# Optimization experiments

Hardware: AMD Instinct MI355X
Metric: run time of the kernel (lower is better)

## Reference

```python
import jax, jax.numpy as jnp
import numpy as np

EPS = 1e-5  # BatchNorm eps (ME.MinkowskiBatchNorm default)


def setup_inputs() -> dict:
    key = jax.random.key(0)
    k1, k2, k3, k4 = jax.random.split(key, 4)
    N, Cin, Cout, K = 65536, 256, 128, 8  # K = kernel_size**dimension = 2**3
    x = jax.random.normal(k1, (N, Cin), dtype=jnp.float32)
    W = jax.random.normal(k2, (K, Cin, Cout), dtype=jnp.float32) * 0.02
    gamma = jax.random.uniform(k3, (Cout,), dtype=jnp.float32, minval=0.5, maxval=1.5)
    beta = jax.random.normal(k4, (Cout,), dtype=jnp.float32) * 0.1
    return {"x": x, "W": W, "gamma": gamma, "beta": beta}


def reference(x, W, gamma, beta):
    # Transpose Minkowski conv, kernel=2, stride=2, dim=3: each input voxel
    # emits 2^3 = 8 disjoint child voxels; child for offset k gets x @ W[k].
    # Kernel map is identity per offset (no scatter-add collisions because
    # kernel_size == stride), so outputs stack to [8*N, Cout].
    Cout = W.shape[-1]
    out = jnp.einsum('nc,kcd->knd', x, W).reshape(-1, Cout)  # [8N, Cout]
    # MinkowskiBatchNorm over all active output sites (training batch stats).
    mean = jnp.mean(out, axis=0)
    var = jnp.mean(jnp.square(out - mean), axis=0)  # biased var, as BN uses
    y = (out - mean) * jax.lax.rsqrt(var + EPS) * gamma + beta
    return jnp.maximum(y, 0.0)  # MinkowskiReLU
```

## Files before the change

### kernel.cpp

```cpp
#include <hip/hip_runtime.h>
#include <stdint.h>

#define N_ROWS 65536
#define CIN 256
#define COUT 128

typedef __bf16 bf16x8 __attribute__((ext_vector_type(8)));
typedef float f32x4 __attribute__((ext_vector_type(4)));
typedef unsigned short u16;
typedef unsigned int u32;

__device__ __forceinline__ float truncbf(float f) {
  u32 x = __builtin_bit_cast(u32, f) & 0xFFFF0000u;
  return __builtin_bit_cast(float, x);
}
__device__ __forceinline__ u32 packbf(float a, float b) {
  return __builtin_amdgcn_perm(__builtin_bit_cast(u32, b),
                               __builtin_bit_cast(u32, a), 0x07060302u);
}
__device__ __forceinline__ u32 bf_rne(float f) {
  u32 u = __builtin_bit_cast(u32, f);
  u += 0x7FFFu + ((u >> 16) & 1);
  return u >> 16;
}

__device__ __forceinline__ void async_ld16(const void* g, void* l) {
  __builtin_amdgcn_global_load_lds((const __attribute__((address_space(1))) u32*)g,
                                   (__attribute__((address_space(3))) u32*)l,
                                   16, 0, 0);
}

template <bool EMIT_XB>
__global__ __launch_bounds__(512, 2) void gram_partial(const float* __restrict__ x,
                                                       u32* __restrict__ part,
                                                       float* __restrict__ csb,
                                                       u32* __restrict__ xb,
                                                       const float* __restrict__ W,
                                                       u16* __restrict__ Wt) {
  __shared__ u32 xT[16 * 260];
  __shared__ float cs_s[8][256];
  __shared__ u16 tile[32][128];
  const int tid = threadIdx.x, lane = tid & 63;
  const int w = tid >> 6;
  const int wm = w >> 2, wn = w & 3;
  const int q = lane >> 4, r = lane & 15;
  const int row0 = blockIdx.x * 256;
  const int cq = tid & 63;
  const int np2 = tid >> 6;

  f32x4 acc[8][4];
  #pragma unroll
  for (int i = 0; i < 8; ++i)
    #pragma unroll
    for (int j = 0; j < 4; ++j) acc[i][j] = (f32x4){0.f, 0.f, 0.f, 0.f};
  f32x4 cs = (f32x4){0.f, 0.f, 0.f, 0.f};

  f32x4 a0, a1, b0, b1;
  {
    const int nA = row0 + np2 * 2;
    const int nB = row0 + (np2 + 8) * 2;
    a0 = *(const f32x4*)&x[(size_t)nA * CIN + 4 * cq];
    a1 = *(const f32x4*)&x[(size_t)(nA + 1) * CIN + 4 * cq];
    b0 = *(const f32x4*)&x[(size_t)nB * CIN + 4 * cq];
    b1 = *(const f32x4*)&x[(size_t)(nB + 1) * CIN + 4 * cq];
  }

  for (int ch = 0; ch < 8; ++ch) {
    const int r0 = row0 + ch * 32;
    const int nA = r0 + np2 * 2;
    const int nB = r0 + (np2 + 8) * 2;

    union { u32 d[4]; uint4 v; } pA, pB;
    #pragma unroll
    for (int j = 0; j < 4; ++j) {
      pA.d[j] = packbf(a0[j], a1[j]);
      pB.d[j] = packbf(b0[j], b1[j]);
      cs[j] += truncbf(a0[j]) + truncbf(a1[j]) + truncbf(b0[j]) + truncbf(b1[j]);
    }
    *(uint4*)&xT[np2 * 260 + 4 * cq] = pA.v;
    *(uint4*)&xT[(np2 + 8) * 260 + 4 * cq] = pB.v;
    if (EMIT_XB) {
      uint2 e;
      e.x = packbf(a0[0], a0[1]); e.y = packbf(a0[2], a0[3]);
      *(uint2*)&xb[(size_t)nA * 128 + 2 * cq] = e;
      e.x = packbf(a1[0], a1[1]); e.y = packbf(a1[2], a1[3]);
      *(uint2*)&xb[(size_t)(nA + 1) * 128 + 2 * cq] = e;
      e.x = packbf(b0[0], b0[1]); e.y = packbf(b0[2], b0[3]);
      *(uint2*)&xb[(size_t)nB * 128 + 2 * cq] = e;
      e.x = packbf(b1[0], b1[1]); e.y = packbf(b1[2], b1[3]);
      *(uint2*)&xb[(size_t)(nB + 1) * 128 + 2 * cq] = e;
    }
    f32x4 na0, na1, nb0, nb1;
    if (ch < 7) {
      const int mA = nA + 32, mB = nB + 32;
      na0 = *(const f32x4*)&x[(size_t)mA * CIN + 4 * cq];
      na1 = *(const f32x4*)&x[(size_t)(mA + 1) * CIN + 4 * cq];
      nb0 = *(const f32x4*)&x[(size_t)mB * CIN + 4 * cq];
      nb1 = *(const f32x4*)&x[(size_t)(mB + 1) * CIN + 4 * cq];
    }
    __syncthreads();
    bf16x8 af[8], bfr[4];
    #pragma unroll
    for (int mt = 0; mt < 8; ++mt) {
      int c = wm * 128 + mt * 16 + r;
      union { u32 d[4]; bf16x8 v; } t;
      #pragma unroll
      for (int s = 0; s < 4; ++s) t.d[s] = xT[(4 * q + s) * 260 + c];
      af[mt] = t.v;
    }
    #pragma unroll
    for (int nt = 0; nt < 4; ++nt) {
      int c = wn * 64 + nt * 16 + r;
      union { u32 d[4]; bf16x8 v; } t;
      #pragma unroll
      for (int s = 0; s < 4; ++s) t.d[s] = xT[(4 * q + s) * 260 + c];
      bfr[nt] = t.v;
    }
    #pragma unroll
    for (int mt = 0; mt < 8; ++mt)
      #pragma unroll
      for (int nt = 0; nt < 4; ++nt)
        acc[mt][nt] = __builtin_amdgcn_mfma_f32_16x16x32_bf16(af[mt], bfr[nt], acc[mt][nt], 0, 0, 0);
    __syncthreads();
    if (ch < 7) { a0 = na0; a1 = na1; b0 = nb0; b1 = nb1; }
  }

  u32* pb = part + (size_t)blockIdx.x * 32768;
  #pragma unroll
  for (int mt = 0; mt < 8; ++mt)
    #pragma unroll
    for (int nt = 0; nt < 4; ++nt) {
      int prow = wm * 64 + mt * 8 + q * 2;
      int col = wn * 64 + nt * 16 + r;
      pb[prow * 256 + col] = (bf_rne(acc[mt][nt][1]) << 16) | bf_rne(acc[mt][nt][0]);
      pb[(prow + 1) * 256 + col] = (bf_rne(acc[mt][nt][3]) << 16) | bf_rne(acc[mt][nt][2]);
    }

  *(f32x4*)&cs_s[np2][4 * cq] = cs;
  __syncthreads();
  if (tid < 256) {
    float s = 0.f;
    #pragma unroll
    for (int p = 0; p < 8; ++p) s += cs_s[p][tid];
    csb[(size_t)blockIdx.x * 256 + tid] = s;
  }

  if (blockIdx.x < 64) {
    const int k = blockIdx.x >> 3, cb = blockIdx.x & 7;
    #pragma unroll
    for (int i = 0; i < 2; ++i) {
      int u = tid + i * 512;
      int ci = u >> 5, d4 = (u & 31) * 4;
      float4 f = *(const float4*)&W[((size_t)k * CIN + cb * 32 + ci) * COUT + d4];
      uint2 p; p.x = packbf(f.x, f.y); p.y = packbf(f.z, f.w);
      *(uint2*)&tile[ci][d4] = p;
    }
    __syncthreads();
    {
      int d = tid >> 2, c0 = (tid & 3) * 8;
      union { u16 s[8]; uint4 u4; } p;
      #pragma unroll
      for (int j = 0; j < 8; ++j) p.s[j] = tile[c0 + j][d];
      *(uint4*)&Wt[((size_t)blockIdx.x * 128 + d) * 32 + c0] = p.u4;
    }
  }
}

__global__ __launch_bounds__(256) void gram_reduce(const u32* __restrict__ part,
                                                   float* __restrict__ G) {
  __shared__ float red[16][128];
  const int t = threadIdx.x;
  const int fi = t & 15, grp = t >> 4;
  const int g0 = blockIdx.x * 64;
  const int rp = g0 >> 8, c0 = g0 & 255;
  float fa[4] = {0.f, 0.f, 0.f, 0.f}, fb[4] = {0.f, 0.f, 0.f, 0.f};
  const u32* p = part + (size_t)(grp * 16) * 32768 + g0 + fi * 4;
  #pragma unroll
  for (int b = 0; b < 16; ++b) {
    uint4 u = *(const uint4*)(p + (size_t)b * 32768);
    const u32* uu = (const u32*)&u;
    #pragma unroll
    for (int j = 0; j < 4; ++j) {
      fa[j] += __builtin_bit_cast(float, uu[j] << 16);
      fb[j] += __builtin_bit_cast(float, uu[j] & 0xFFFF0000u);
    }
  }
  #pragma unroll
  for (int j = 0; j < 4; ++j) {
    float2 v; v.x = fa[j]; v.y = fb[j];
    *(float2*)&red[grp][(fi * 4 + j) * 2] = v;
  }
  __syncthreads();
  if (t < 128) {
    int ci = t & 63, par = t >> 6;
    float s = 0.f;
    #pragma unroll
    for (int g = 0; g < 16; ++g) s += red[g][ci * 2 + par];
    G[(size_t)(2 * rp + par) * 256 + c0 + ci] = s;
  }
}

__global__ __launch_bounds__(256) void stats_kernel(const float* __restrict__ G,
                                                    const float* __restrict__ csb,
                                                    const float* __restrict__ W,
                                                    const float* __restrict__ gamma,
                                                    const float* __restrict__ beta,
                                                    float* __restrict__ scale,
                                                    float* __restrict__ bias) {
  const int d = blockIdx.x;
  const int t = threadIdx.x;
  __shared__ float wv[256][8];
  __shared__ float rr[16];
  float cst = 0.f;
  for (int b = 0; b < 256; ++b) cst += csb[b * 256 + t];
  float wt[8];
  #pragma unroll
  for (int k = 0; k < 8; ++k) wt[k] = truncbf(W[((size_t)k * CIN + t) * COUT + d]);
  #pragma unroll
  for (int k = 0; k < 8; ++k) wv[t][k] = wt[k];
  __syncthreads();

  float q = 0.f;
  for (int j = 0; j < 256; ++j) {
    float g = G[j * 256 + t];
    float dot = 0.f;
    #pragma unroll
    for (int k = 0; k < 8; ++k) dot += wv[j][k] * wt[k];
    q += g * dot;
  }
  float wsum = 0.f;
  #pragma unroll
  for (int k = 0; k < 8; ++k) wsum += wt[k];
  float m = cst * wsum;

  #pragma unroll
  for (int off = 32; off; off >>= 1) {
    q += __shfl_down(q, off, 64);
    m += __shfl_down(m, off, 64);
  }
  int wid = t >> 6;
  if ((t & 63) == 0) { rr[wid] = q; rr[wid + 8] = m; }
  __syncthreads();
  if (t == 0) {
    float qt = rr[0] + rr[1] + rr[2] + rr[3];
    float mn = rr[8] + rr[9] + rr[10] + rr[11];
    const float invM = 1.f / 524288.f;
    float mean = mn * invM;
    float var = qt * invM - mean * mean;
    float s = gamma[d] * rsqrtf(var + 1e-5f);
    scale[d] = s;
    bias[d] = beta[d] - mean * s;
  }
}

__global__ __launch_bounds__(256, 2) void gemm_xb(const u16* __restrict__ xb,
                                                  const u16* __restrict__ Wt,
                                                  const float* __restrict__ scale,
                                                  const float* __restrict__ bias,
                                                  float* __restrict__ out) {
  __shared__ u16 As[32768];
  const int tid = threadIdx.x, lane = tid & 63;
  const int w = tid >> 6, wr = w >> 1, wc = w & 1;
  const int q = lane >> 4, r = lane & 15;
  const int m0 = blockIdx.x * 128;

  #pragma unroll
  for (int i = 0; i < 16; ++i) {
    int u = tid + i * 256;
    int cb = u >> 9, row = (u >> 2) & 127;
    int sseg = (u ^ (u >> 3)) & 3;
    const u16* g = xb + (size_t)(m0 + row) * CIN + cb * 32 + sseg * 8;
    async_ld16(g, As + (size_t)u * 8);
  }

  float sv[4], bv[4];
  #pragma unroll
  for (int nt = 0; nt < 4; ++nt) {
    int col = wc * 64 + nt * 16 + r;
    sv[nt] = scale[col]; bv[nt] = bias[col];
  }

  const int boff = (wc * 64 + r) * 32 + q * 8;
  const int sw = (q ^ ((r >> 1) & 3)) * 8;
  bf16x8 bcur[4], bnext[4];
  #pragma unroll
  for (int nt = 0; nt < 4; ++nt)
    bcur[nt] = *(const bf16x8*)&Wt[boff + nt * 512];

  __syncthreads();

  int j = 0;
  for (int k = 0; k < 8; ++k) {
    f32x4 acc[4][4];
    #pragma unroll
    for (int i = 0; i < 4; ++i)
      #pragma unroll
      for (int jj = 0; jj < 4; ++jj) acc[i][jj] = (f32x4){0.f, 0.f, 0.f, 0.f};

    #pragma unroll
    for (int cb = 0; cb < 8; ++cb) {
      if (j < 63) {
        #pragma unroll
        for (int nt = 0; nt < 4; ++nt)
          bnext[nt] = *(const bf16x8*)&Wt[(size_t)(j + 1) * 4096 + boff + nt * 512];
      }
      bf16x8 af[4];
      #pragma unroll
      for (int mt = 0; mt < 4; ++mt)
        af[mt] = *(const bf16x8*)&As[((cb * 128) + wr * 64 + mt * 16 + r) * 32 + sw];
      #pragma unroll
      for (int mt = 0; mt < 4; ++mt)
        #pragma unroll
        for (int nt = 0; nt < 4; ++nt)
          acc[mt][nt] = __builtin_amdgcn_mfma_f32_16x16x32_bf16(af[mt], bcur[nt], acc[mt][nt], 0, 0, 0);
      if (j < 63) {
        #pragma unroll
        for (int nt = 0; nt < 4; ++nt) bcur[nt] = bnext[nt];
      }
      ++j;
    }

    const size_t obase = (size_t)k * N_ROWS + m0;
    #pragma unroll
    for (int mt = 0; mt < 4; ++mt)
      #pragma unroll
      for (int nt = 0; nt < 4; ++nt)
        #pragma unroll
        for (int i = 0; i < 4; ++i) {
          int grow = wr * 64 + mt * 16 + q * 4 + i;
          int col = wc * 64 + nt * 16 + r;
          float y = acc[mt][nt][i] * sv[nt] + bv[nt];
          y = y > 0.f ? y : 0.f;
          out[(obase + grow) * COUT + col] = y;
        }
  }
}

__global__ __launch_bounds__(256, 2) void gemm_fp32(const float* __restrict__ x,
                                                    const u16* __restrict__ Wt,
                                                    const float* __restrict__ scale,
                                                    const float* __restrict__ bias,
                                                    float* __restrict__ out) {
  __shared__ float Asf[4096];
  const int tid = threadIdx.x, lane = tid & 63;
  const int w = tid >> 6, wr = w >> 1, wc = w & 1;
  const int q = lane >> 4, r = lane & 15;
  const int k = blockIdx.x & 7;
  const int m0 = (blockIdx.x >> 3) * 128;

  const u16* wbase = Wt + (size_t)k * 8 * 4096;
  const int boff = (wc * 64 + r) * 32 + q * 8;

  bf16x8 bcur[4], bnext[4];
  #pragma unroll
  for (int nt = 0; nt < 4; ++nt)
    bcur[nt] = *(const bf16x8*)&wbase[boff + nt * 512];

  f32x4 acc[4][4];
  #pragma unroll
  for (int i = 0; i < 4; ++i)
    #pragma unroll
    for (int j = 0; j < 4; ++j) acc[i][j] = (f32x4){0.f, 0.f, 0.f, 0.f};

  for (int cb = 0; cb < 8; ++cb) {
    #pragma unroll
    for (int i = 0; i < 4; ++i) {
      int u = tid + i * 256;
      int row = u >> 3;
      int s = (u & 7) ^ (row & 7);
      const float* g = x + (size_t)(m0 + row) * CIN + cb * 32 + s * 4;
      async_ld16(g, Asf + (w * 64 + i * 256) * 4);
    }
    if (cb < 7) {
      #pragma unroll
      for (int nt = 0; nt < 4; ++nt)
        bnext[nt] = *(const bf16x8*)&wbase[(cb + 1) * 4096 + boff + nt * 512];
    }
    __syncthreads();
    bf16x8 af[4];
    #pragma unroll
    for (int mt = 0; mt < 4; ++mt) {
      int row = wr * 64 + mt * 16 + r;
      union { u32 d[4]; bf16x8 v; } t;
      #pragma unroll
      for (int b = 0; b < 2; ++b) {
        int unit = row * 8 + ((2 * q + b) ^ (row & 7));
        float4 f = *(const float4*)&Asf[unit * 4];
        t.d[b * 2 + 0] = packbf(f.x, f.y);
        t.d[b * 2 + 1] = packbf(f.z, f.w);
      }
      af[mt] = t.v;
    }
    #pragma unroll
    for (int mt = 0; mt < 4; ++mt)
      #pragma unroll
      for (int nt = 0; nt < 4; ++nt)
        acc[mt][nt] = __builtin_amdgcn_mfma_f32_16x16x32_bf16(af[mt], bcur[nt], acc[mt][nt], 0, 0, 0);
    __syncthreads();
    if (cb < 7) {
      #pragma unroll
      for (int nt = 0; nt < 4; ++nt) bcur[nt] = bnext[nt];
    }
  }

  float sv[4], bv[4];
  #pragma unroll
  for (int nt = 0; nt < 4; ++nt) {
    int col = wc * 64 + nt * 16 + r;
    sv[nt] = scale[col]; bv[nt] = bias[col];
  }
  const size_t obase = (size_t)k * N_ROWS + m0;
  #pragma unroll
  for (int mt = 0; mt < 4; ++mt)
    #pragma unroll
    for (int nt = 0; nt < 4; ++nt)
      #pragma unroll
      for (int i = 0; i < 4; ++i) {
        int grow = wr * 64 + mt * 16 + q * 4 + i;
        int col = wc * 64 + nt * 16 + r;
        float y = acc[mt][nt][i] * sv[nt] + bv[nt];
        y = y > 0.f ? y : 0.f;
        out[(obase + grow) * COUT + col] = y;
      }
}

extern "C" void kernel_launch(void* const* d_in, const int* in_sizes, int n_in,
                              void* d_out, int out_size, void* d_ws, size_t ws_size,
                              hipStream_t stream) {
  const float* x = (const float*)d_in[0];
  const float* W = (const float*)d_in[1];
  const float* gamma = (const float*)d_in[2];
  const float* beta = (const float*)d_in[3];
  float* out = (float*)d_out;

  float* ws = (float*)d_ws;
  float* G = ws;
  float* csb = ws + 65536;
  float* scale = ws + 131072;
  float* bias = ws + 131200;
  u16* Wt = (u16*)(ws + 131328);
  u32* xb = (u32*)((char*)d_ws + (2u << 20));
  const size_t need = (2u << 20) + (size_t)N_ROWS * CIN * 2;
  const bool big_ws = ws_size >= need;

  u32* part = (u32*)d_out;

  if (big_ws) {
    gram_partial<true><<<256, 512, 0, stream>>>(x, part, csb, xb, W, Wt);
  } else {
    gram_partial<false><<<256, 512, 0, stream>>>(x, part, csb, xb, W, Wt);
  }
  gram_reduce<<<512, 256, 0, stream>>>(part, G);
  stats_kernel<<<128, 256, 0, stream>>>(G, csb, W, gamma, beta, scale, bias);
  if (big_ws) {
    gemm_xb<<<512, 256, 0, stream>>>((const u16*)xb, Wt, scale, bias, out);
  } else {
    gemm_fp32<<<4096, 256, 0, stream>>>(x, Wt, scale, bias, out);
  }
}
```

Before: 383.2 us.

## Drop bf16 x copy, convert fp32 x in GEMM, halve gram grid

The gram pass no longer writes a bf16 copy of x to workspace. The output GEMM now loads fp32 x directly and packs it to bf16 in registers before storing to LDS, and the fp32 async fallback kernel is removed. Separately, gram_partial now processes 512 rows per block with 128 blocks, which halves the partial Gram buffers and the reduce and column-sum work. The aim is to remove the extra write and read of the bf16 intermediate. In exchange, the GEMM reads twice as many bytes of x per tile and converts synchronously, and the gram stage runs with fewer blocks.

Result: no change. 379.6 us (-0.9%).

```diff
diff --git a/kernel.cpp b/kernel.cpp
--- a/kernel.cpp
+++ b/kernel.cpp
@@ -24,17 +24,9 @@
   return u >> 16;
 }
 
-__device__ __forceinline__ void async_ld16(const void* g, void* l) {
-  __builtin_amdgcn_global_load_lds((const __attribute__((address_space(1))) u32*)g,
-                                   (__attribute__((address_space(3))) u32*)l,
-                                   16, 0, 0);
-}
-
-template <bool EMIT_XB>
 __global__ __launch_bounds__(512, 2) void gram_partial(const float* __restrict__ x,
                                                        u32* __restrict__ part,
                                                        float* __restrict__ csb,
-                                                       u32* __restrict__ xb,
                                                        const float* __restrict__ W,
                                                        u16* __restrict__ Wt) {
   __shared__ u32 xT[16 * 260];
@@ -44,7 +36,7 @@
   const int w = tid >> 6;
   const int wm = w >> 2, wn = w & 3;
   const int q = lane >> 4, r = lane & 15;
-  const int row0 = blockIdx.x * 256;
+  const int row0 = blockIdx.x * 512;
   const int cq = tid & 63;
   const int np2 = tid >> 6;
 
@@ -65,11 +57,7 @@
     b1 = *(const f32x4*)&x[(size_t)(nB + 1) * CIN + 4 * cq];
   }
 
-  for (int ch = 0; ch < 8; ++ch) {
-    const int r0 = row0 + ch * 32;
-    const int nA = r0 + np2 * 2;
-    const int nB = r0 + (np2 + 8) * 2;
-
+  for (int ch = 0; ch < 16; ++ch) {
     union { u32 d[4]; uint4 v; } pA, pB;
     #pragma unroll
     for (int j = 0; j < 4; ++j) {
@@ -79,20 +67,12 @@
     }
     *(uint4*)&xT[np2 * 260 + 4 * cq] = pA.v;
     *(uint4*)&xT[(np2 + 8) * 260 + 4 * cq] = pB.v;
-    if (EMIT_XB) {
-      uint2 e;
-      e.x = packbf(a0[0], a0[1]); e.y = packbf(a0[2], a0[3]);
-      *(uint2*)&xb[(size_t)nA * 128 + 2 * cq] = e;
-      e.x = packbf(a1[0], a1[1]); e.y = packbf(a1[2], a1[3]);
-      *(uint2*)&xb[(size_t)(nA + 1) * 128 + 2 * cq] = e;
-      e.x = packbf(b0[0], b0[1]); e.y = packbf(b0[2], b0[3]);
-      *(uint2*)&xb[(size_t)nB * 128 + 2 * cq] = e;
-      e.x = packbf(b1[0], b1[1]); e.y = packbf(b1[2], b1[3]);
-      *(uint2*)&xb[(size_t)(nB + 1) * 128 + 2 * cq] = e;
-    }
+
     f32x4 na0, na1, nb0, nb1;
-    if (ch < 7) {
-      const int mA = nA + 32, mB = nB + 32;
+    if (ch < 15) {
+      const int r0n = row0 + (ch + 1) * 32;
+      const int mA = r0n + np2 * 2;
+      const int mB = r0n + (np2 + 8) * 2;
       na0 = *(const f32x4*)&x[(size_t)mA * CIN + 4 * cq];
       na1 = *(const f32x4*)&x[(size_t)(mA + 1) * CIN + 4 * cq];
       nb0 = *(const f32x4*)&x[(size_t)mB * CIN + 4 * cq];
@@ -122,7 +102,7 @@
       for (int nt = 0; nt < 4; ++nt)
         acc[mt][nt] = __builtin_amdgcn_mfma_f32_16x16x32_bf16(af[mt], bfr[nt], acc[mt][nt], 0, 0, 0);
     __syncthreads();
-    if (ch < 7) { a0 = na0; a1 = na1; b0 = nb0; b1 = nb1; }
+    if (ch < 15) { a0 = na0; a1 = na1; b0 = nb0; b1 = nb1; }
   }
 
   u32* pb = part + (size_t)blockIdx.x * 32768;
@@ -174,9 +154,9 @@
   const int g0 = blockIdx.x * 64;
   const int rp = g0 >> 8, c0 = g0 & 255;
   float fa[4] = {0.f, 0.f, 0.f, 0.f}, fb[4] = {0.f, 0.f, 0.f, 0.f};
-  const u32* p = part + (size_t)(grp * 16) * 32768 + g0 + fi * 4;
-  #pragma unroll
-  for (int b = 0; b < 16; ++b) {
+  const u32* p = part + (size_t)(grp * 8) * 32768 + g0 + fi * 4;
+  #pragma unroll
+  for (int b = 0; b < 8; ++b) {
     uint4 u = *(const uint4*)(p + (size_t)b * 32768);
     const u32* uu = (const u32*)&u;
     #pragma unroll
@@ -212,7 +192,7 @@
   __shared__ float wv[256][8];
   __shared__ float rr[16];
   float cst = 0.f;
-  for (int b = 0; b < 256; ++b) cst += csb[b * 256 + t];
+  for (int b = 0; b < 128; ++b) cst += csb[b * 256 + t];
   float wt[8];
   #pragma unroll
   for (int k = 0; k < 8; ++k) wt[k] = truncbf(W[((size_t)k * CIN + t) * COUT + d]);
@@ -253,11 +233,11 @@
   }
 }
 
-__global__ __launch_bounds__(256, 2) void gemm_xb(const u16* __restrict__ xb,
-                                                  const u16* __restrict__ Wt,
-                                                  const float* __restrict__ scale,
-                                                  const float* __restrict__ bias,
-                                                  float* __restrict__ out) {
+__global__ __launch_bounds__(256, 2) void gemm_x(const float* __restrict__ x,
+                                                 const u16* __restrict__ Wt,
+                                                 const float* __restrict__ scale,
+                                                 const float* __restrict__ bias,
+                                                 float* __restrict__ out) {
   __shared__ u16 As[32768];
   const int tid = threadIdx.x, lane = tid & 63;
   const int w = tid >> 6, wr = w >> 1, wc = w & 1;
@@ -269,8 +249,15 @@
     int u = tid + i * 256;
     int cb = u >> 9, row = (u >> 2) & 127;
     int sseg = (u ^ (u >> 3)) & 3;
-    const u16* g = xb + (size_t)(m0 + row) * CIN + cb * 32 + sseg * 8;
-    async_ld16(g, As + (size_t)u * 8);
+    const float* g = &x[(size_t)(m0 + row) * CIN + cb * 32 + sseg * 8];
+    f32x4 f0 = *(const f32x4*)g;
+    f32x4 f1 = *(const f32x4*)(g + 4);
+    union { u32 d[4]; uint4 v; } t4;
+    t4.d[0] = packbf(f0[0], f0[1]);
+    t4.d[1] = packbf(f0[2], f0[3]);
+    t4.d[2] = packbf(f1[0], f1[1]);
+    t4.d[3] = packbf(f1[2], f1[3]);
+    *(uint4*)&As[(size_t)u * 8] = t4.v;
   }
 
   float sv[4], bv[4];
@@ -336,94 +323,6 @@
   }
 }
 
-__global__ __launch_bounds__(256, 2) void gemm_fp32(const float* __restrict__ x,
-                                                    const u16* __restrict__ Wt,
-                                                    const float* __restrict__ scale,
-                                                    const float* __restrict__ bias,
-                                                    float* __restrict__ out) {
-  __shared__ float Asf[4096];
-  const int tid = threadIdx.x, lane = tid & 63;
-  const int w = tid >> 6, wr = w >> 1, wc = w & 1;
-  const int q = lane >> 4, r = lane & 15;
-  const int k = blockIdx.x & 7;
-  const int m0 = (blockIdx.x >> 3) * 128;
-
-  const u16* wbase = Wt + (size_t)k * 8 * 4096;
-  const int boff = (wc * 64 + r) * 32 + q * 8;
-
-  bf16x8 bcur[4], bnext[4];
-  #pragma unroll
-  for (int nt = 0; nt < 4; ++nt)
-    bcur[nt] = *(const bf16x8*)&wbase[boff + nt * 512];
-
-  f32x4 acc[4][4];
-  #pragma unroll
-  for (int i = 0; i < 4; ++i)
-    #pragma unroll
-    for (int j = 0; j < 4; ++j) acc[i][j] = (f32x4){0.f, 0.f, 0.f, 0.f};
-
-  for (int cb = 0; cb < 8; ++cb) {
-    #pragma unroll
-    for (int i = 0; i < 4; ++i) {
-      int u = tid + i * 256;
-      int row = u >> 3;
-      int s = (u & 7) ^ (row & 7);
-      const float* g = x + (size_t)(m0 + row) * CIN + cb * 32 + s * 4;
-      async_ld16(g, Asf + (w * 64 + i * 256) * 4);
-    }
-    if (cb < 7) {
-      #pragma unroll
-      for (int nt = 0; nt < 4; ++nt)
-        bnext[nt] = *(const bf16x8*)&wbase[(cb + 1) * 4096 + boff + nt * 512];
-    }
-    __syncthreads();
-    bf16x8 af[4];
-    #pragma unroll
-    for (int mt = 0; mt < 4; ++mt) {
-      int row = wr * 64 + mt * 16 + r;
-      union { u32 d[4]; bf16x8 v; } t;
-      #pragma unroll
-      for (int b = 0; b < 2; ++b) {
-        int unit = row * 8 + ((2 * q + b) ^ (row & 7));
-        float4 f = *(const float4*)&Asf[unit * 4];
-        t.d[b * 2 + 0] = packbf(f.x, f.y);
-        t.d[b * 2 + 1] = packbf(f.z, f.w);
-      }
-      af[mt] = t.v;
-    }
-    #pragma unroll
-    for (int mt = 0; mt < 4; ++mt)
-      #pragma unroll
-      for (int nt = 0; nt < 4; ++nt)
-        acc[mt][nt] = __builtin_amdgcn_mfma_f32_16x16x32_bf16(af[mt], bcur[nt], acc[mt][nt], 0, 0, 0);
-    __syncthreads();
-    if (cb < 7) {
-      #pragma unroll
-      for (int nt = 0; nt < 4; ++nt) bcur[nt] = bnext[nt];
-    }
-  }
-
-  float sv[4], bv[4];
-  #pragma unroll
-  for (int nt = 0; nt < 4; ++nt) {
-    int col = wc * 64 + nt * 16 + r;
-    sv[nt] = scale[col]; bv[nt] = bias[col];
-  }
-  const size_t obase = (size_t)k * N_ROWS + m0;
-  #pragma unroll
-  for (int mt = 0; mt < 4; ++mt)
-    #pragma unroll
-    for (int nt = 0; nt < 4; ++nt)
-      #pragma unroll
-      for (int i = 0; i < 4; ++i) {
-        int grow = wr * 64 + mt * 16 + q * 4 + i;
-        int col = wc * 64 + nt * 16 + r;
-        float y = acc[mt][nt][i] * sv[nt] + bv[nt];
-        y = y > 0.f ? y : 0.f;
-        out[(obase + grow) * COUT + col] = y;
-      }
-}
-
 extern "C" void kernel_launch(void* const* d_in, const int* in_sizes, int n_in,
                               void* d_out, int out_size, void* d_ws, size_t ws_size,
                               hipStream_t stream) {
@@ -436,25 +335,14 @@
   float* ws = (float*)d_ws;
   float* G = ws;
   float* csb = ws + 65536;
-  float* scale = ws + 131072;
-  float* bias = ws + 131200;
-  u16* Wt = (u16*)(ws + 131328);
-  u32* xb = (u32*)((char*)d_ws + (2u << 20));
-  const size_t need = (2u << 20) + (size_t)N_ROWS * CIN * 2;
-  const bool big_ws = ws_size >= need;
+  float* scale = ws + 98304;
+  float* bias = ws + 98432;
+  u16* Wt = (u16*)(ws + 98560);
 
   u32* part = (u32*)d_out;
 
-  if (big_ws) {
-    gram_partial<true><<<256, 512, 0, stream>>>(x, part, csb, xb, W, Wt);
-  } else {
-    gram_partial<false><<<256, 512, 0, stream>>>(x, part, csb, xb, W, Wt);
-  }
+  gram_partial<<<128, 512, 0, stream>>>(x, part, csb, W, Wt);
   gram_reduce<<<512, 256, 0, stream>>>(part, G);
   stats_kernel<<<128, 256, 0, stream>>>(G, csb, W, gamma, beta, scale, bias);
-  if (big_ws) {
-    gemm_xb<<<512, 256, 0, stream>>>((const u16*)xb, Wt, scale, bias, out);
-  } else {
-    gemm_fp32<<<4096, 256, 0, stream>>>(x, Wt, scale, bias, out);
-  }
-}
+  gemm_x<<<512, 256, 0, stream>>>(x, Wt, scale, bias, out);
+}
```
